# Performance work log

Hardware: AMD Instinct MI355X
Metric: run time of the kernel (lower is better)

Reference implementation:

```python
import jax, jax.numpy as jnp
import numpy as np

HIDDEN = 1024
NUM_HEADS = 16
HEAD_DIM = HIDDEN // NUM_HEADS  # 64
GRID_SIZE = 5
SPLINE_ORDER = 3
GRID_LO, GRID_HI = -1.0, 1.0


def b_splines(x2d, grid, k=SPLINE_ORDER):
    # x2d: (N, in), grid: (in, GRID_SIZE + 2k + 1) -> (N, in, GRID_SIZE + k)
    xg = x2d[:, :, None]
    g = grid[None, :, :]
    bases = ((xg >= g[:, :, :-1]) & (xg < g[:, :, 1:])).astype(x2d.dtype)
    for j in range(1, k + 1):
        left = (xg - g[:, :, : -(j + 1)]) / (g[:, :, j:-1] - g[:, :, : -(j + 1)]) * bases[:, :, :-1]
        right = (g[:, :, j + 1 :] - xg) / (g[:, :, j + 1 :] - g[:, :, 1:-j]) * bases[:, :, 1:]
        bases = left + right
    return bases


def setup_inputs() -> dict:
    key = jax.random.key(0)
    ks = jax.random.split(key, 6)
    B, S = 1, 2048
    in_f, out_f = HIDDEN, 3 * HIDDEN
    x = jax.random.normal(ks[0], (B, S, HIDDEN), dtype=jnp.float32)
    base_weight = jax.random.normal(ks[1], (out_f, in_f), dtype=jnp.float32) * (1.0 / np.sqrt(in_f))
    n_coef = GRID_SIZE + SPLINE_ORDER  # 8
    spline_weight = jax.random.normal(ks[2], (out_f, in_f, n_coef), dtype=jnp.float32) * 0.1
    spline_scaler = jnp.ones((out_f, in_f), dtype=jnp.float32)
    out_w = jax.random.normal(ks[3], (HIDDEN, HIDDEN), dtype=jnp.float32) * (1.0 / np.sqrt(HIDDEN))
    out_b = jnp.zeros((HIDDEN,), dtype=jnp.float32)
    # extended B-spline grid, same for every input feature
    h = (GRID_HI - GRID_LO) / GRID_SIZE
    grid_row = jnp.arange(-SPLINE_ORDER, GRID_SIZE + SPLINE_ORDER + 1, dtype=jnp.float32) * h + GRID_LO
    grid = jnp.tile(grid_row[None, :], (in_f, 1))  # (in, GRID_SIZE + 2k + 1)
    # RoPE rotation matrix (cos/sin of pos * theta), theta base 10000
    half = HEAD_DIM // 2
    inv_freq = 1.0 / (10000.0 ** (jnp.arange(0, half, dtype=jnp.float32) / half))
    angles = jnp.arange(S, dtype=jnp.float32)[:, None] * inv_freq[None, :]  # (S, half)
    rot_cos = jnp.cos(angles)
    rot_sin = jnp.sin(angles)
    return {"x": x, "base_weight": base_weight, "spline_weight": spline_weight,
            "spline_scaler": spline_scaler, "out_w": out_w, "out_b": out_b,
            "grid": grid, "rot_cos": rot_cos, "rot_sin": rot_sin}


def apply_rope(t, rot_cos, rot_sin):
    # t: (B, H, S, D); pairs (t[..., 2i], t[..., 2i+1]) viewed as complex, mult by cis
    tr = t[..., 0::2]
    ti = t[..., 1::2]
    c = rot_cos[None, None, :, :]
    s = rot_sin[None, None, :, :]
    nr = tr * c - ti * s
    ni = tr * s + ti * c
    return jnp.stack([nr, ni], axis=-1).reshape(t.shape)


def reference(x, base_weight, spline_weight, spline_scaler, out_w, out_b, grid, rot_cos, rot_sin):
    B, S, H = x.shape
    N = B * S
    x2 = x.reshape(N, H)
    # KANLinear: base branch + spline branch
    base = jax.nn.silu(x2) @ base_weight.T  # (N, 3H)
    bs = b_splines(x2, grid)  # (N, in, G+k)
    sw = (spline_weight * spline_scaler[:, :, None]).reshape(spline_weight.shape[0], -1)
    spline = bs.reshape(N, -1) @ sw.T
    qkv = (base + spline).reshape(B, S, NUM_HEADS, 3 * HEAD_DIM).transpose(0, 2, 1, 3)
    q, k, v = jnp.split(qkv, 3, axis=-1)  # each (B, nh, S, hd)
    q = apply_rope(q, rot_cos, rot_sin)
    k = apply_rope(k, rot_cos, rot_sin)
    scores = jnp.einsum("bhqd,bhkd->bhqk", q, k) / np.sqrt(HEAD_DIM).astype(np.float32)
    attn = jax.nn.softmax(scores, axis=-1)
    ctx = jnp.einsum("bhqk,bhkd->bhqd", attn, v)
    ctx = ctx.transpose(0, 2, 1, 3).reshape(B, S, H)
    return ctx @ out_w.T + out_b
```

## Files before the change

kernel.cpp:

```cpp
#include <hip/hip_runtime.h>

#define DEVI __device__ __forceinline__

typedef float f32x4 __attribute__((ext_vector_type(4)));
typedef __bf16 bf16x8 __attribute__((ext_vector_type(8)));

constexpr int S   = 2048;
constexpr int HID = 1024;
constexpr int HD  = 64;
constexpr int O3  = 3072;
constexpr int KF  = 9216;

DEVI unsigned short f2bf(float f) {
  unsigned int u = __float_as_uint(f);
  u = (u + 0x7FFFu + ((u >> 16) & 1u)) >> 16;
  return (unsigned short)u;
}
DEVI float b2f(unsigned int u) { return __uint_as_float(u << 16); }
DEVI float fexp(float x) { return __builtin_amdgcn_exp2f(x * 1.44269504089f); }

DEVI void gload16(const void* g, void* l) {
  __builtin_amdgcn_global_load_lds((const __attribute__((address_space(1))) void*)g,
                                   (__attribute__((address_space(3))) void*)l, 16, 0, 0);
}

#define BAR() asm volatile("s_barrier" ::: "memory")
#define VMC0() asm volatile("s_waitcnt vmcnt(0)" ::: "memory")
#define VMC2() asm volatile("s_waitcnt vmcnt(2)" ::: "memory")

__global__ __launch_bounds__(256) void kconv_w(const float* __restrict__ bw,
    const float* __restrict__ sw, const float* __restrict__ sc,
    unsigned short* __restrict__ Wc) {
  unsigned int t = blockIdx.x * 256 + threadIdx.x;
  unsigned int o = t / 1152, jc = t % 1152;
  unsigned int j = jc * 8;
  float v[8];
  if (j < 1024) {
    const float4* p = (const float4*)(bw + (size_t)o * 1024 + j);
    float4 a = p[0], b = p[1];
    v[0]=a.x; v[1]=a.y; v[2]=a.z; v[3]=a.w; v[4]=b.x; v[5]=b.y; v[6]=b.z; v[7]=b.w;
  } else {
    unsigned int i = (j - 1024) >> 3;
    float s = sc[(size_t)o * 1024 + i];
    const float4* p = (const float4*)(sw + ((size_t)o * 1024 + i) * 8);
    float4 a = p[0], b = p[1];
    v[0]=a.x*s; v[1]=a.y*s; v[2]=a.z*s; v[3]=a.w*s; v[4]=b.x*s; v[5]=b.y*s; v[6]=b.z*s; v[7]=b.w*s;
  }
  union { unsigned short u[8]; uint4 q; } pk;
  #pragma unroll
  for (int c = 0; c < 8; ++c) pk.u[c] = f2bf(v[c]);
  *(uint4*)(Wc + (size_t)o * KF + j) = pk.q;
}

__global__ __launch_bounds__(256) void kconv_outw(const float* __restrict__ ow,
    unsigned short* __restrict__ Wo) {
  unsigned int t = blockIdx.x * 256 + threadIdx.x;
  unsigned int o = t >> 7, j = (t & 127) * 8;
  const float4* p = (const float4*)(ow + (size_t)o * 1024 + j);
  float4 a = p[0], b = p[1];
  float v[8] = {a.x, a.y, a.z, a.w, b.x, b.y, b.z, b.w};
  union { unsigned short u[8]; uint4 q; } pk;
  #pragma unroll
  for (int c = 0; c < 8; ++c) pk.u[c] = f2bf(v[c]);
  *(uint4*)(Wo + (size_t)o * 1024 + j) = pk.q;
}

__global__ __launch_bounds__(256) void kfeatures(const float* __restrict__ x,
    const float* __restrict__ grid, unsigned short* __restrict__ F) {
  unsigned int t = blockIdx.x * 256 + threadIdx.x;
  unsigned int n = t >> 10, i = t & 1023;
  float xv = x[t];
  float sil = xv / (1.f + expf(-xv));
  F[(size_t)n * KF + i] = f2bf(sil);
  float g[12];
  #pragma unroll
  for (int j = 0; j < 12; ++j) g[j] = grid[j];
  float b[11];
  #pragma unroll
  for (int j = 0; j < 11; ++j) b[j] = (xv >= g[j] && xv < g[j + 1]) ? 1.f : 0.f;
  #pragma unroll
  for (int ord = 1; ord <= 3; ++ord) {
    float inv[11];
    #pragma unroll
    for (int a = 0; a + ord < 12 && a < 11; ++a) {
      float d = g[a + ord] - g[a];
      float r = __builtin_amdgcn_rcpf(d);
      inv[a] = r * (2.f - d * r);
    }
    #pragma unroll
    for (int j = 0; j + ord < 11; ++j)
      b[j] = (xv - g[j]) * inv[j] * b[j]
           + (g[j + ord + 1] - xv) * inv[j + 1] * b[j + 1];
  }
  union { unsigned short u[8]; uint4 q; } pk;
  #pragma unroll
  for (int c = 0; c < 8; ++c) pk.u[c] = f2bf(b[c]);
  *(uint4*)(F + (size_t)n * KF + 1024 + i * 8) = pk.q;
}

__global__ __launch_bounds__(512) void kgemm256(const unsigned short* __restrict__ A,
    const unsigned short* __restrict__ W, unsigned short* __restrict__ C) {
  int lin = blockIdx.x + (blockIdx.y << 3) + (blockIdx.z << 7);
  int swz = (lin & 7) * 32 + (lin >> 3);
  int kz = swz >> 7;
  int r = swz & 127;
  int bm = r >> 4, bn = r & 15;
  const int tid = threadIdx.x;
  const int wid = tid >> 6;
  const int lane = tid & 63;
  const int l16 = lane & 15, g4 = lane >> 4;
  const int wr = wid >> 2, wc = wid & 3;
  const int koff = kz * 72;

  __shared__ __align__(16) unsigned short As[2][2][128 * 64];
  __shared__ __align__(16) unsigned short Bs[2][192 * 64];

  const size_t rA0 = (size_t)bm * 256;
  const size_t rB0 = (size_t)bn * 192;

  auto stageA = [&](int buf, int half, int t) {
    const unsigned short* src = A + (rA0 + half * 128) * (size_t)KF + (size_t)(koff + t) * 64;
    char* lds = (char*)As[buf][half];
    #pragma unroll
    for (int rr = 0; rr < 2; ++rr) {
      int chunk = rr * 512 + tid;
      int row = chunk >> 3;
      int c8 = (chunk & 7) ^ (row & 7);
      gload16(src + (size_t)row * KF + c8 * 8, lds + (rr * 512 + wid * 64) * 16);
    }
  };
  auto stageB = [&](int buf, int third, int t) {
    const unsigned short* src = W + (rB0 + third * 64) * (size_t)KF + (size_t)(koff + t) * 64;
    char* lds = (char*)Bs[buf] + third * 8192;
    int row = tid >> 3;
    int c8 = (tid & 7) ^ (row & 7);
    gload16(src + (size_t)row * KF + c8 * 8, lds + (wid * 64) * 16);
  };

  f32x4 acc[8][3] = {};
  bf16x8 bb[3][2];

#define GPH(Q, BUF, STMTS, DOVM) do {                                          \
    bf16x8 ar[2][2];                                                           \
    _Pragma("unroll") for (int f = 0; f < 2; ++f)                              \
      _Pragma("unroll") for (int ks = 0; ks < 2; ++ks) {                       \
        int rw = (2 * (Q) + f) * 16 + l16;                                     \
        ar[f][ks] = *(const bf16x8*)(As[BUF][wr] + rw * 64 +                   \
                                     (((ks * 4 + g4) ^ (l16 & 7)) * 8));       \
      }                                                                        \
    if ((Q) == 0) {                                                            \
      _Pragma("unroll") for (int fb = 0; fb < 3; ++fb)                         \
        _Pragma("unroll") for (int ks = 0; ks < 2; ++ks) {                     \
          int rw = wc * 48 + fb * 16 + l16;                                    \
          bb[fb][ks] = *(const bf16x8*)(Bs[BUF] + rw * 64 +                    \
                                        (((ks * 4 + g4) ^ (l16 & 7)) * 8));    \
        }                                                                      \
    }                                                                          \
    STMTS;                                                                     \
    if (DOVM) VMC2();                                                          \
    BAR();                                                                     \
    __builtin_amdgcn_s_setprio(1);                                             \
    _Pragma("unroll") for (int f = 0; f < 2; ++f)                              \
      _Pragma("unroll") for (int fb = 0; fb < 3; ++fb)                         \
        _Pragma("unroll") for (int ks = 0; ks < 2; ++ks)                       \
          acc[2 * (Q) + f][fb] = __builtin_amdgcn_mfma_f32_16x16x32_bf16(      \
              ar[f][ks], bb[fb][ks], acc[2 * (Q) + f][fb], 0, 0, 0);           \
    __builtin_amdgcn_s_setprio(0);                                             \
    BAR();                                                                     \
  } while (0)

  stageB(0, 0, 0); stageB(0, 1, 0); stageB(0, 2, 0);
  stageA(0, 0, 0); stageA(0, 1, 0);
  stageB(1, 0, 1); stageB(1, 1, 1); stageB(1, 2, 1);
  VMC0();
  BAR();

  for (int it = 0; it < 36; ++it) {
    int t0 = 2 * it;
    int tA1 = t0 + 1;
    int tN0 = t0 + 2 < 72 ? t0 + 2 : 71;
    int tN1 = t0 + 3 < 72 ? t0 + 3 : 71;
    GPH(0, 0, { stageA(1, 0, tA1); }, 0);
    GPH(1, 0, { stageA(1, 1, tA1); stageB(0, 0, tN0); }, 0);
    GPH(2, 0, { stageB(0, 1, tN0); }, 0);
    GPH(3, 0, { stageB(0, 2, tN0); }, 1);
    GPH(0, 1, { stageA(0, 0, tN0); }, 0);
    GPH(1, 1, { stageA(0, 1, tN0); stageB(1, 0, tN1); }, 0);
    GPH(2, 1, { stageB(1, 1, tN1); }, 0);
    GPH(3, 1, { stageB(1, 2, tN1); }, 1);
  }
#undef GPH

  unsigned short* Cb = C + (size_t)kz * 2048 * 3072;
  #pragma unroll
  for (int fr = 0; fr < 8; ++fr) {
    int rowb = bm * 256 + wr * 128 + fr * 16 + g4 * 4;
    #pragma unroll
    for (int fb = 0; fb < 3; ++fb) {
      int col = bn * 192 + wc * 48 + fb * 16 + l16;
      #pragma unroll
      for (int rg = 0; rg < 4; ++rg)
        Cb[(size_t)(rowb + rg) * 3072 + col] = f2bf(acc[fr][fb][rg]);
    }
  }
}

__global__ __launch_bounds__(256) void kgemm_bt(const unsigned short* __restrict__ A,
    const unsigned short* __restrict__ W, float* __restrict__ C,
    const float* __restrict__ bias, int N, int nkPer) {
  const int bm = blockIdx.x, bn = blockIdx.y;
  const int tid = threadIdx.x;
  const int w = tid >> 6, lane = tid & 63;
  const int l16 = lane & 15, g4 = lane >> 4;
  const int wr = w >> 1, wcc = w & 1;
  __shared__ __align__(16) unsigned short As[2][128 * 32];
  __shared__ __align__(16) unsigned short Bs[2][128 * 32];
  f32x4 acc[4][4] = {};
  const int K = 1024;

  auto STAGE = [&](int buf, int kt) {
    #pragma unroll
    for (int r = 0; r < 2; ++r) {
      int chunk = r * 256 + w * 64 + lane;
      int row = chunk >> 2, col = (chunk & 3) * 8;
      int ldsoff = (r * 256 + w * 64) * 16;
      gload16(A + (size_t)(bm * 128 + row) * K + kt * 32 + col, (char*)As[buf] + ldsoff);
      gload16(W + (size_t)(bn * 128 + row) * K + kt * 32 + col, (char*)Bs[buf] + ldsoff);
    }
  };

  STAGE(0, 0);
  VMC0();
  BAR();
  int cur = 0;
  for (int kt = 0; kt < nkPer; ++kt) {
    if (kt + 1 < nkPer) STAGE(cur ^ 1, kt + 1);
    bf16x8 af[4], bfr[4];
    #pragma unroll
    for (int f = 0; f < 4; ++f)
      af[f] = *(const bf16x8*)(As[cur] + (wr * 64 + f * 16 + l16) * 32 + g4 * 8);
    #pragma unroll
    for (int f = 0; f < 4; ++f)
      bfr[f] = *(const bf16x8*)(Bs[cur] + (wcc * 64 + f * 16 + l16) * 32 + g4 * 8);
    __builtin_amdgcn_s_setprio(1);
    #pragma unroll
    for (int fr = 0; fr < 4; ++fr)
      #pragma unroll
      for (int fc = 0; fc < 4; ++fc)
        acc[fr][fc] = __builtin_amdgcn_mfma_f32_16x16x32_bf16(af[fr], bfr[fc], acc[fr][fc], 0, 0, 0);
    __builtin_amdgcn_s_setprio(0);
    VMC0();
    BAR();
    cur ^= 1;
  }
  #pragma unroll
  for (int fr = 0; fr < 4; ++fr) {
    int rowb = bm * 128 + wr * 64 + fr * 16 + g4 * 4;
    #pragma unroll
    for (int fc = 0; fc < 4; ++fc) {
      int col = bn * 128 + wcc * 64 + fc * 16 + l16;
      float bv = bias[col];
      #pragma unroll
      for (int rg = 0; rg < 4; ++rg)
        C[(size_t)(rowb + rg) * N + col] = acc[fr][fc][rg] + bv;
    }
  }
}

__global__ __launch_bounds__(256) void krope_qk(const unsigned short* __restrict__ qp,
    int splits, const float* __restrict__ rc, const float* __restrict__ rs,
    unsigned short* __restrict__ Qb, unsigned short* __restrict__ Kb) {
  unsigned int t = blockIdx.x * 256 + threadIdx.x;
  int d = t & 31;
  int h = (t >> 5) & 15;
  int n = t >> 9;
  float qr = 0.f, qi = 0.f, kr = 0.f, ki = 0.f;
  for (int p = 0; p < splits; ++p) {
    size_t base = (size_t)p * 2048 * O3 + (size_t)n * O3 + h * 192;
    unsigned int a = *(const unsigned int*)(qp + base + 2 * d);
    unsigned int e = *(const unsigned int*)(qp + base + 64 + 2 * d);
    qr += b2f(a & 0xffffu); qi += b2f(a >> 16);
    kr += b2f(e & 0xffffu); ki += b2f(e >> 16);
  }
  float c = rc[n * 32 + d], sn = rs[n * 32 + d];
  unsigned int qpk = (unsigned int)f2bf((qr * c - qi * sn) * 0.125f)
                   | ((unsigned int)f2bf((qr * sn + qi * c) * 0.125f) << 16);
  unsigned int kpk = (unsigned int)f2bf(kr * c - ki * sn)
                   | ((unsigned int)f2bf(kr * sn + ki * c) << 16);
  *(unsigned int*)(Qb + (size_t)h * S * HD + (size_t)n * HD + 2 * d) = qpk;
  *(unsigned int*)(Kb + (size_t)h * S * HD + (size_t)n * HD + 2 * d) = kpk;
}

__global__ __launch_bounds__(256) void kpack_vt(const unsigned short* __restrict__ qp,
    int splits, unsigned short* __restrict__ Vt) {
  const int nt = blockIdx.x;
  const int h  = blockIdx.y;
  const int tid = threadIdx.x;
  __shared__ __align__(16) unsigned short T[64][72];
  const int n0 = nt * 64;
  #pragma unroll
  for (int it = 0; it < 2; ++it) {
    int idx = it * 256 + tid;
    int r = idx >> 3;
    int c8 = (idx & 7) * 8;
    float acc[8] = {};
    for (int p = 0; p < splits; ++p) {
      size_t base = (size_t)p * 2048 * O3 + (size_t)(n0 + r) * O3 + h * 192 + 128 + c8;
      uint4 u = *(const uint4*)(qp + base);
      const unsigned short* pu = (const unsigned short*)&u;
      #pragma unroll
      for (int j = 0; j < 8; ++j) acc[j] += b2f(pu[j]);
    }
    #pragma unroll
    for (int j = 0; j < 8; ++j) T[c8 + j][r] = f2bf(acc[j]);
  }
  __syncthreads();
  #pragma unroll
  for (int it = 0; it < 2; ++it) {
    int idx = it * 256 + tid;
    int dd = idx >> 3;
    int c8 = (idx & 7) * 8;
    *(uint4*)(Vt + (size_t)h * HD * S + (size_t)dd * S + n0 + c8) = *(const uint4*)&T[dd][c8];
  }
}

__global__ __launch_bounds__(256) void kattn(const unsigned short* __restrict__ Qb,
    const unsigned short* __restrict__ Kb, const unsigned short* __restrict__ Vt,
    unsigned short* __restrict__ ctx) {
  const int qb = blockIdx.x, h = blockIdx.y;
  const int tid = threadIdx.x, w = tid >> 6, lane = tid & 63;
  const int l16 = lane & 15, g4 = lane >> 4;
  __shared__ __align__(16) unsigned short Ks[2][64 * 64];
  __shared__ __align__(16) unsigned short Vs[2][64 * 64];
  __shared__ __align__(16) unsigned short Ps[4][16 * 64];
  const unsigned short* Qh = Qb + (size_t)h * S * HD;
  const unsigned short* Kh = Kb + (size_t)h * S * HD;
  const unsigned short* Vh = Vt + (size_t)h * HD * S;
  bf16x8 qf[2];
  #pragma unroll
  for (int ks = 0; ks < 2; ++ks)
    qf[ks] = *(const bf16x8*)(Qh + (size_t)(qb * 64 + w * 16 + l16) * HD + ks * 32 + g4 * 8);
  f32x4 o[4] = {};
  float lp[4] = {0.f, 0.f, 0.f, 0.f};

  auto STAGE = [&](int buf, int t) {
    int kv0 = t * 64;
    #pragma unroll
    for (int r = 0; r < 2; ++r) {
      int chunk = r * 256 + w * 64 + lane;
      int row = chunk >> 3;
      int c8 = ((chunk ^ row) & 7) * 8;
      int ldsoff = (r * 256 + w * 64) * 16;
      gload16(Kh + (size_t)(kv0 + row) * HD + c8, (char*)Ks[buf] + ldsoff);
      gload16(Vh + (size_t)row * S + kv0 + c8, (char*)Vs[buf] + ldsoff);
    }
  };

  STAGE(0, 0);
  VMC0();
  BAR();
  int cur = 0;
  for (int t = 0; t < S / 64; ++t) {
    if (t + 1 < S / 64) STAGE(cur ^ 1, t + 1);
    const unsigned short* Kc = Ks[cur];
    const unsigned short* Vc = Vs[cur];
    f32x4 s[4] = {};
    __builtin_amdgcn_s_setprio(1);
    #pragma unroll
    for (int fc = 0; fc < 4; ++fc) {
      int rw = fc * 16 + l16;
      #pragma unroll
      for (int ks = 0; ks < 2; ++ks) {
        bf16x8 bk = *(const bf16x8*)(Kc + rw * 64 + (((ks * 4 + g4) ^ (l16 & 7)) * 8));
        s[fc] = __builtin_amdgcn_mfma_f32_16x16x32_bf16(qf[ks], bk, s[fc], 0, 0, 0);
      }
    }
    __builtin_amdgcn_s_setprio(0);
    #pragma unroll
    for (int fc = 0; fc < 4; ++fc)
      #pragma unroll
      for (int rg = 0; rg < 4; ++rg) {
        float p = fexp(s[fc][rg]);
        lp[rg] += p;
        int row = g4 * 4 + rg;
        Ps[w][row * 64 + ((fc * 2 + (l16 >> 3)) ^ (row & 7)) * 8 + (l16 & 7)] = f2bf(p);
      }
    __builtin_amdgcn_s_setprio(1);
    #pragma unroll
    for (int ks = 0; ks < 2; ++ks) {
      bf16x8 ap = *(const bf16x8*)(Ps[w] + l16 * 64 + (((ks * 4 + g4) ^ (l16 & 7)) * 8));
      #pragma unroll
      for (int fc = 0; fc < 4; ++fc) {
        int rw = fc * 16 + l16;
        bf16x8 bv = *(const bf16x8*)(Vc + rw * 64 + (((ks * 4 + g4) ^ (l16 & 7)) * 8));
        o[fc] = __builtin_amdgcn_mfma_f32_16x16x32_bf16(ap, bv, o[fc], 0, 0, 0);
      }
    }
    __builtin_amdgcn_s_setprio(0);
    VMC0();
    BAR();
    cur ^= 1;
  }
  #pragma unroll
  for (int rg = 0; rg < 4; ++rg) {
    float l = lp[rg];
    l += __shfl_xor(l, 1, 64);
    l += __shfl_xor(l, 2, 64);
    l += __shfl_xor(l, 4, 64);
    l += __shfl_xor(l, 8, 64);
    float inv = 1.f / l;
    int row = qb * 64 + w * 16 + g4 * 4 + rg;
    #pragma unroll
    for (int fc = 0; fc < 4; ++fc)
      ctx[(size_t)row * HID + h * HD + fc * 16 + l16] = f2bf(o[fc][rg] * inv);
  }
}

extern "C" void kernel_launch(void* const* d_in, const int* in_sizes, int n_in,
                              void* d_out, int out_size, void* d_ws, size_t ws_size,
                              hipStream_t stream) {
  const float* x    = (const float*)d_in[0];
  const float* bw   = (const float*)d_in[1];
  const float* sw   = (const float*)d_in[2];
  const float* sc   = (const float*)d_in[3];
  const float* ow   = (const float*)d_in[4];
  const float* ob   = (const float*)d_in[5];
  const float* grid = (const float*)d_in[6];
  const float* rc   = (const float*)d_in[7];
  const float* rs   = (const float*)d_in[8];
  float* out = (float*)d_out;
  char* ws = (char*)d_ws;

  const int splits = 2;

  unsigned short* F    = (unsigned short*)(ws);
  unsigned short* Wc   = (unsigned short*)(ws + 37748736);
  unsigned short* Wo   = (unsigned short*)(ws + 94371840);
  unsigned short* qkvp = (unsigned short*)(ws + 96468992);
  char* tail = ws + 96468992 + (size_t)splits * 12582912;
  unsigned short* Qb   = (unsigned short*)(tail);
  unsigned short* Kb   = (unsigned short*)(tail + 4194304);
  unsigned short* Vt   = (unsigned short*)(tail + 8388608);
  unsigned short* ctx  = (unsigned short*)(tail + 12582912);

  kconv_w   <<<dim3(13824), dim3(256), 0, stream>>>(bw, sw, sc, Wc);
  kconv_outw<<<dim3(512),   dim3(256), 0, stream>>>(ow, Wo);
  kfeatures <<<dim3(8192),  dim3(256), 0, stream>>>(x, grid, F);
  kgemm256  <<<dim3(8, 16, 2), dim3(512), 0, stream>>>(F, Wc, qkvp);
  krope_qk  <<<dim3(4096),  dim3(256), 0, stream>>>(qkvp, splits, rc, rs, Qb, Kb);
  kpack_vt  <<<dim3(32, 16), dim3(256), 0, stream>>>(qkvp, splits, Vt);
  kattn     <<<dim3(32, 16), dim3(256), 0, stream>>>(Qb, Kb, Vt, ctx);
  kgemm_bt  <<<dim3(16, 8),  dim3(256), 0, stream>>>(ctx, Wo, out, ob, 1024, 32);
}
```

Baseline: 421.6 us.

## Triple-buffer A tiles in KAN GEMM to deepen prefetch pipeline

Changes the A-operand shared-memory staging in the 256x192 bf16 GEMM from double to triple buffering with rotating buffer indices. A tiles are now prefetched two k-steps ahead, and the wait count is relaxed from vmcnt(2) to vmcnt(7) so more global loads stay in flight across barriers. This targets load latency stalls in the main loop, at the cost of more LDS per block (fewer resident blocks possible) and extra index bookkeeping.

```diff
diff --git a/kernel.cpp b/kernel.cpp
--- a/kernel.cpp
+++ b/kernel.cpp
@@ -26,7 +26,7 @@
 
 #define BAR() asm volatile("s_barrier" ::: "memory")
 #define VMC0() asm volatile("s_waitcnt vmcnt(0)" ::: "memory")
-#define VMC2() asm volatile("s_waitcnt vmcnt(2)" ::: "memory")
+#define VMC7() asm volatile("s_waitcnt vmcnt(7)" ::: "memory")
 
 __global__ __launch_bounds__(256) void kconv_w(const float* __restrict__ bw,
     const float* __restrict__ sw, const float* __restrict__ sc,
@@ -112,15 +112,16 @@
   const int wr = wid >> 2, wc = wid & 3;
   const int koff = kz * 72;
 
-  __shared__ __align__(16) unsigned short As[2][2][128 * 64];
+  __shared__ __align__(16) unsigned short As[3][256 * 64];
   __shared__ __align__(16) unsigned short Bs[2][192 * 64];
 
   const size_t rA0 = (size_t)bm * 256;
   const size_t rB0 = (size_t)bn * 192;
 
   auto stageA = [&](int buf, int half, int t) {
+    if (t > 71) t = 71;
     const unsigned short* src = A + (rA0 + half * 128) * (size_t)KF + (size_t)(koff + t) * 64;
-    char* lds = (char*)As[buf][half];
+    char* lds = (char*)&As[buf][0] + half * 16384;
     #pragma unroll
     for (int rr = 0; rr < 2; ++rr) {
       int chunk = rr * 512 + tid;
@@ -130,8 +131,9 @@
     }
   };
   auto stageB = [&](int buf, int third, int t) {
+    if (t > 71) t = 71;
     const unsigned short* src = W + (rB0 + third * 64) * (size_t)KF + (size_t)(koff + t) * 64;
-    char* lds = (char*)Bs[buf] + third * 8192;
+    char* lds = (char*)&Bs[buf][0] + third * 8192;
     int row = tid >> 3;
     int c8 = (tid & 7) ^ (row & 7);
     gload16(src + (size_t)row * KF + c8 * 8, lds + (wid * 64) * 16);
@@ -140,24 +142,24 @@
   f32x4 acc[8][3] = {};
   bf16x8 bb[3][2];
 
-#define GPH(Q, BUF, STMTS, DOVM) do {                                          \
+#define GPH(Q, ABUF, BBUF, STMTS, DOVM) do {                                   \
     bf16x8 ar[2][2];                                                           \
     _Pragma("unroll") for (int f = 0; f < 2; ++f)                              \
       _Pragma("unroll") for (int ks = 0; ks < 2; ++ks) {                       \
-        int rw = (2 * (Q) + f) * 16 + l16;                                     \
-        ar[f][ks] = *(const bf16x8*)(As[BUF][wr] + rw * 64 +                   \
+        int rw = wr * 128 + (2 * (Q) + f) * 16 + l16;                          \
+        ar[f][ks] = *(const bf16x8*)(&As[ABUF][0] + rw * 64 +                  \
                                      (((ks * 4 + g4) ^ (l16 & 7)) * 8));       \
       }                                                                        \
     if ((Q) == 0) {                                                            \
       _Pragma("unroll") for (int fb = 0; fb < 3; ++fb)                         \
         _Pragma("unroll") for (int ks = 0; ks < 2; ++ks) {                     \
           int rw = wc * 48 + fb * 16 + l16;                                    \
-          bb[fb][ks] = *(const bf16x8*)(Bs[BUF] + rw * 64 +                    \
+          bb[fb][ks] = *(const bf16x8*)(&Bs[BBUF][0] + rw * 64 +               \
                                         (((ks * 4 + g4) ^ (l16 & 7)) * 8));    \
         }                                                                      \
     }                                                                          \
     STMTS;                                                                     \
-    if (DOVM) VMC2();                                                          \
+    if (DOVM) VMC7();                                                          \
     BAR();                                                                     \
     __builtin_amdgcn_s_setprio(1);                                             \
     _Pragma("unroll") for (int f = 0; f < 2; ++f)                              \
@@ -169,27 +171,29 @@
     BAR();                                                                     \
   } while (0)
 
+  stageA(0, 0, 0); stageA(0, 1, 0);
   stageB(0, 0, 0); stageB(0, 1, 0); stageB(0, 2, 0);
-  stageA(0, 0, 0); stageA(0, 1, 0);
+  stageA(1, 0, 1); stageA(1, 1, 1);
   stageB(1, 0, 1); stageB(1, 1, 1); stageB(1, 2, 1);
   VMC0();
   BAR();
 
+  int a0 = 0, a1 = 1, a2 = 2;
+  #pragma unroll 3
   for (int it = 0; it < 36; ++it) {
     int t0 = 2 * it;
-    int tA1 = t0 + 1;
-    int tN0 = t0 + 2 < 72 ? t0 + 2 : 71;
-    int tN1 = t0 + 3 < 72 ? t0 + 3 : 71;
-    GPH(0, 0, { stageA(1, 0, tA1); }, 0);
-    GPH(1, 0, { stageA(1, 1, tA1); stageB(0, 0, tN0); }, 0);
-    GPH(2, 0, { stageB(0, 1, tN0); }, 0);
-    GPH(3, 0, { stageB(0, 2, tN0); }, 1);
-    GPH(0, 1, { stageA(0, 0, tN0); }, 0);
-    GPH(1, 1, { stageA(0, 1, tN0); stageB(1, 0, tN1); }, 0);
-    GPH(2, 1, { stageB(1, 1, tN1); }, 0);
-    GPH(3, 1, { stageB(1, 2, tN1); }, 1);
+    GPH(0, a0, 0, { stageA(a2, 0, t0 + 2); }, 0);
+    GPH(1, a0, 0, { stageA(a2, 1, t0 + 2); stageB(0, 0, t0 + 2); }, 0);
+    GPH(2, a0, 0, { stageB(0, 1, t0 + 2); }, 0);
+    GPH(3, a0, 0, { stageB(0, 2, t0 + 2); }, 1);
+    GPH(0, a1, 1, { stageA(a0, 0, t0 + 3); }, 0);
+    GPH(1, a1, 1, { stageA(a0, 1, t0 + 3); stageB(1, 0, t0 + 3); }, 0);
+    GPH(2, a1, 1, { stageB(1, 1, t0 + 3); }, 0);
+    GPH(3, a1, 1, { stageB(1, 2, t0 + 3); }, 1);
+    int tmp = a0; a0 = a2; a2 = a1; a1 = tmp;
   }
 #undef GPH
+  VMC0();
 
   unsigned short* Cb = C + (size_t)kz * 2048 * 3072;
   #pragma unroll
```

New measurement: 420.2 us. No clear change (-0.3%).
